# Performance work log

Measured on AMD Instinct MI355X. Metric: run time of the kernel, lower is better.

## Reference

```python
import jax, jax.numpy as jnp
import numpy as np

N, E = 50000, 800000
IN_F, HID_F, OUT_F = 128, 128, 32


def setup_inputs() -> dict:
    key = jax.random.key(0)
    ks = jax.random.split(key, 16)
    glorot = lambda k, i, o: jax.random.normal(k, (i, o), jnp.float32) * (2.0 / (i + o)) ** 0.5
    return {
        "x": jax.random.normal(ks[0], (N, IN_F), jnp.float32),
        "src": jax.random.randint(ks[1], (E,), 0, N, jnp.int64),
        "dst": jax.random.randint(ks[2], (E,), 0, N, jnp.int64),
        # layer 0: mean aggregator
        "W_self0": glorot(ks[3], IN_F, HID_F),
        "W_neigh0": glorot(ks[4], IN_F, HID_F),
        "b0": jnp.zeros((HID_F,), jnp.float32),
        # layers 1,2: gcn aggregator (fc_neigh only)
        "W_neigh1": glorot(ks[5], HID_F, HID_F),
        "b1": jnp.zeros((HID_F,), jnp.float32),
        "W_neigh2": glorot(ks[6], HID_F, HID_F),
        "b2": jnp.zeros((HID_F,), jnp.float32),
        # layer 3: mean aggregator
        "W_self3": glorot(ks[7], HID_F, OUT_F),
        "W_neigh3": glorot(ks[8], HID_F, OUT_F),
        "b3": jnp.zeros((OUT_F,), jnp.float32),
    }


def _l2_normalize(x, eps=1e-12):
    # torch F.normalize(x): x / max(||x||_2, eps) along dim 1
    n = jnp.sqrt(jnp.sum(x * x, axis=1, keepdims=True))
    return x / jnp.maximum(n, eps)


def _agg_sum(h, src, dst, n):
    # sum of in-neighbor (src) features onto dst nodes: [N, d]
    return jax.ops.segment_sum(h[src], dst, num_segments=n)


def _sage_mean(h, src, dst, deg, W_self, W_neigh, b):
    nbr = _agg_sum(h, src, dst, h.shape[0]) / jnp.maximum(deg, 1.0)[:, None]
    return h @ W_self + nbr @ W_neigh + b


def _sage_gcn(h, src, dst, deg, W_neigh, b):
    hn = (_agg_sum(h, src, dst, h.shape[0]) + h) / (deg + 1.0)[:, None]
    return hn @ W_neigh + b


def reference(x, src, dst, W_self0, W_neigh0, b0, W_neigh1, b1, W_neigh2, b2,
              W_self3, W_neigh3, b3):
    n = x.shape[0]
    deg = jax.ops.segment_sum(jnp.ones_like(dst, jnp.float32), dst, num_segments=n)
    h = _l2_normalize(x)
    h = jax.nn.relu(_sage_mean(h, src, dst, deg, W_self0, W_neigh0, b0))
    h = jax.nn.relu(_sage_gcn(h, src, dst, deg, W_neigh1, b1))
    h = jax.nn.relu(_sage_gcn(h, src, dst, deg, W_neigh2, b2))
    h = _sage_mean(h, src, dst, deg, W_self3, W_neigh3, b3)  # no relu on last layer
    return h
```

## Files before the change

kernel.cpp:

```cpp
#include <hip/hip_runtime.h>

#define NN 50000
#define NE 800000
#define F  128
#define FO 32

#define RSH  8
#define RSZ  256
#define NBKT 196
#define CAP  5120
#define PCHUNK 4096
#define NPB  ((NE + PCHUNK - 1) / PCHUNK)
#define LGRID ((NN + 3) / 4)

typedef _Float16 h16;
typedef h16   half8 __attribute__((ext_vector_type(8)));
typedef h16   h16x4 __attribute__((ext_vector_type(4)));
typedef h16   h16x2 __attribute__((ext_vector_type(2)));
typedef float f32x4 __attribute__((ext_vector_type(4)));

__device__ __forceinline__ void wprep_one(const float* __restrict__ W,
        h16* __restrict__ Wf, int idx, int NC, int NCT) {
    if (idx >= 128 * NC) return;
    int k = idx / NC, n = idx - k * NC;
    int kt = k >> 5, g = (k & 31) >> 3, j = k & 7;
    int ct = n >> 4;
    int lane = g * 16 + (n & 15);
    float w = W[idx];
    h16 hi = (h16)w;
    h16 lo = (h16)(w - (float)hi);
    int base = ((kt * NCT + ct) * 64 + lane) * 8 + j;
    Wf[base] = hi;
    Wf[base + NCT * 2048] = lo;
}

__global__ __launch_bounds__(256) void k_pre0(
        const float* __restrict__ S0, const float* __restrict__ N0,
        const float* __restrict__ N1, const float* __restrict__ N2,
        const float* __restrict__ S3, const float* __restrict__ N3,
        h16* fS0, h16* fN0, h16* fN1, h16* fN2, h16* fS3, h16* fN3,
        int* __restrict__ bcur) {
    int bb = blockIdx.x, tid = threadIdx.x;
    if (bb < 256) {
        const float* W = bb < 64 ? S0 : bb < 128 ? N0 : bb < 192 ? N1 : N2;
        h16*        Wf = bb < 64 ? fS0 : bb < 128 ? fN0 : bb < 192 ? fN1 : fN2;
        wprep_one(W, Wf, (bb & 63) * 256 + tid, 128, 8);
    } else if (bb < 288) {
        int b2 = bb - 256;
        const float* W = b2 < 16 ? S3 : N3;
        h16*        Wf = b2 < 16 ? fS3 : fN3;
        wprep_one(W, Wf, (b2 & 15) * 256 + tid, 32, 2);
    } else {
        if (tid < NBKT) bcur[tid] = 0;
    }
}

__global__ __launch_bounds__(256) void k_pre1(const int* __restrict__ src,
        const int* __restrict__ dst, int* __restrict__ bcur, int* __restrict__ barea,
        const float* __restrict__ x, h16* __restrict__ hhi, h16* __restrict__ hlo) {
    __shared__ int cnt[NBKT];
    __shared__ int base[NBKT];
    const int tid = threadIdx.x;
    if ((int)blockIdx.x < NPB) {
        const int e0 = blockIdx.x * PCHUNK;
        for (int i = tid; i < NBKT; i += 256) cnt[i] = 0;
        __syncthreads();
        #pragma unroll
        for (int k = 0; k < PCHUNK / 256; ++k) {
            int e = e0 + k * 256 + tid;
            if (e < NE) atomicAdd(&cnt[dst[e] >> RSH], 1);
        }
        __syncthreads();
        for (int i = tid; i < NBKT; i += 256)
            base[i] = atomicAdd(&bcur[i], cnt[i]);
        __syncthreads();
        for (int i = tid; i < NBKT; i += 256) cnt[i] = base[i];
        __syncthreads();
        #pragma unroll
        for (int k = 0; k < PCHUNK / 256; ++k) {
            int e = e0 + k * 256 + tid;
            if (e < NE) {
                int d = dst[e], s = src[e];
                int b = d >> RSH;
                int p = atomicAdd(&cnt[b], 1);
                barea[b * CAP + p] = ((d & (RSZ - 1)) << 16) | s;
            }
        }
    } else {
        const int bb   = blockIdx.x - NPB;
        const int wid  = bb * 4 + (tid >> 6);
        const int lane = tid & 63;
        if (wid >= NN) return;
        const float2* xr = (const float2*)(x + (size_t)wid * F);
        float2 v = xr[lane];
        float ss = v.x * v.x + v.y * v.y;
        #pragma unroll
        for (int d = 1; d < 64; d <<= 1) ss += __shfl_xor(ss, d, 64);
        float inv = 1.0f / fmaxf(sqrtf(ss), 1e-12f);
        float ox = v.x * inv, oy = v.y * inv;
        h16 hx = (h16)ox, hy = (h16)oy;
        h16x2 vhi = {hx, hy};
        h16x2 vlo = {(h16)(ox - (float)hx), (h16)(oy - (float)hy)};
        *(h16x2*)(hhi + (size_t)wid * F + lane * 2) = vhi;
        *(h16x2*)(hlo + (size_t)wid * F + lane * 2) = vlo;
    }
}

__global__ __launch_bounds__(256) void k_bfill(const int* __restrict__ barea,
        const int* __restrict__ bcur, int* __restrict__ offs,
        float* __restrict__ degf, int* __restrict__ csr) {
    __shared__ int pre[NBKT];
    __shared__ int hist_cur[RSZ];
    __shared__ int ws[4];
    const int r = blockIdx.x, tid = threadIdx.x;
    const int lane = tid & 63, wv = tid >> 6;
    int bv = (tid < NBKT) ? bcur[tid] : 0;
    int bi = bv;
    #pragma unroll
    for (int d = 1; d < 64; d <<= 1) {
        int t = __shfl_up(bi, d, 64);
        if (lane >= d) bi += t;
    }
    if (lane == 63) ws[wv] = bi;
    __syncthreads();
    if (tid == 0) {
        int run = 0;
        #pragma unroll
        for (int w = 0; w < 4; ++w) { int t = ws[w]; ws[w] = run; run += t; }
    }
    __syncthreads();
    if (tid < NBKT) pre[tid] = ws[wv] + bi - bv;
    if (r == 0 && tid == NBKT - 1) offs[NN] = ws[wv] + bi;
    __syncthreads();
    const int nb    = bcur[r];
    const int gbase = pre[r];
    const int node  = (r << RSH) + tid;
    hist_cur[tid] = 0;
    __syncthreads();
    const int* area = barea + r * CAP;
    for (int i = tid; i < nb; i += 256) atomicAdd(&hist_cur[area[i] >> 16], 1);
    __syncthreads();
    const int v = hist_cur[tid];
    int incl = v;
    #pragma unroll
    for (int d = 1; d < 64; d <<= 1) {
        int t = __shfl_up(incl, d, 64);
        if (lane >= d) incl += t;
    }
    __syncthreads();
    if (lane == 63) ws[wv] = incl;
    __syncthreads();
    if (tid == 0) {
        int run = 0;
        #pragma unroll
        for (int w = 0; w < 4; ++w) { int t = ws[w]; ws[w] = run; run += t; }
    }
    __syncthreads();
    const int ex = ws[wv] + incl - v;
    if (node < NN) {
        offs[node] = gbase + ex;
        degf[node] = (float)v;
    }
    __syncthreads();
    hist_cur[tid] = gbase + ex;
    __syncthreads();
    for (int i = tid; i < nb; i += 256) {
        int pk = area[i];
        int p = atomicAdd(&hist_cur[pk >> 16], 1);
        csr[p] = pk & 0xFFFF;
    }
}

template<int NCT, bool OUT16>
__device__ __forceinline__ void mfma_cols(const half8* Ahi, const half8* Alo,
        const h16* __restrict__ Wf, void* __restrict__ out, int row0, int l) {
    const int cdc = l & 15;
    const int cdr = (l >> 4) * 4;
    #pragma unroll
    for (int ct = 0; ct < NCT; ++ct) {
        f32x4 acc = {0.f, 0.f, 0.f, 0.f};
        #pragma unroll
        for (int kt = 0; kt < 4; ++kt) {
            half8 bh = *(const half8*)(Wf + (size_t)(((kt * NCT + ct) * 64 + l) * 8));
            half8 bl = *(const half8*)(Wf + (size_t)((((4 + kt) * NCT + ct) * 64 + l) * 8));
            acc = __builtin_amdgcn_mfma_f32_16x16x32_f16(Ahi[kt], bh, acc, 0, 0, 0);
            acc = __builtin_amdgcn_mfma_f32_16x16x32_f16(Alo[kt], bh, acc, 0, 0, 0);
            acc = __builtin_amdgcn_mfma_f32_16x16x32_f16(Ahi[kt], bl, acc, 0, 0, 0);
        }
        #pragma unroll
        for (int r = 0; r < 4; ++r) {
            int gr = row0 + cdr + r;
            if (gr < NN) {
                size_t oi = (size_t)gr * (NCT * 16) + ct * 16 + cdc;
                if constexpr (OUT16) ((h16*)out)[oi] = (h16)acc[r];
                else                 ((float*)out)[oi] = acc[r];
            }
        }
    }
}

template<int NCTA, int NCTB, bool A16, bool B16>
__global__ __launch_bounds__(256) void k_mfma(const h16* __restrict__ hhi,
        const h16* __restrict__ hlo, const h16* __restrict__ WfA,
        const h16* __restrict__ WfB, void* __restrict__ outA,
        void* __restrict__ outB) {
    const int tid = threadIdx.x;
    const int l   = tid & 63;
    const int wv  = tid >> 6;
    const int row0 = blockIdx.x * 64 + wv * 16;
    int ar = row0 + (l & 15); if (ar >= NN) ar = NN - 1;
    const size_t ab = (size_t)ar * F + (l >> 4) * 8;
    half8 Ahi[4], Alo[4];
    #pragma unroll
    for (int kt = 0; kt < 4; ++kt) {
        Ahi[kt] = *(const half8*)(hhi + ab + kt * 32);
        Alo[kt] = *(const half8*)(hlo + ab + kt * 32);
    }
    mfma_cols<NCTA, A16>(Ahi, Alo, WfA, outA, row0, l);
    if constexpr (NCTB > 0) mfma_cols<NCTB, B16>(Ahi, Alo, WfB, outB, row0, l);
}

template<int MODE>
__global__ __launch_bounds__(256) void k_agg128(const h16* __restrict__ g,
        const h16* __restrict__ s, const int* __restrict__ offs,
        const int* __restrict__ csr, const float* __restrict__ degf,
        const float* __restrict__ b, h16* __restrict__ hhi, h16* __restrict__ hlo) {
    const int wid  = (int)((blockIdx.x * 256 + threadIdx.x) >> 6);
    const int lane = threadIdx.x & 63;
    if (wid >= NN) return;
    const int q  = lane >> 4;
    const int li = lane & 15;
    const int beg = offs[wid], end = offs[wid + 1];
    const half8* g8 = (const half8*)g;
    float a0[8], a1[8];
    #pragma unroll
    for (int j = 0; j < 8; ++j) { a0[j] = 0.f; a1[j] = 0.f; }
    int e = beg;
    for (; e + 16 <= end; e += 16) {
        int u0 = csr[e + q];
        int u1 = csr[e + 4 + q];
        int u2 = csr[e + 8 + q];
        int u3 = csr[e + 12 + q];
        half8 v0 = g8[(size_t)u0 * 16 + li];
        half8 v1 = g8[(size_t)u1 * 16 + li];
        half8 v2 = g8[(size_t)u2 * 16 + li];
        half8 v3 = g8[(size_t)u3 * 16 + li];
        #pragma unroll
        for (int j = 0; j < 8; ++j) {
            a0[j] += (float)v0[j] + (float)v2[j];
            a1[j] += (float)v1[j] + (float)v3[j];
        }
    }
    for (; e + 4 <= end; e += 4) {
        half8 v = g8[(size_t)csr[e + q] * 16 + li];
        #pragma unroll
        for (int j = 0; j < 8; ++j) a0[j] += (float)v[j];
    }
    if (q < end - e) {
        half8 v = g8[(size_t)csr[e + q] * 16 + li];
        #pragma unroll
        for (int j = 0; j < 8; ++j) a1[j] += (float)v[j];
    }
    #pragma unroll
    for (int j = 0; j < 8; ++j) {
        a0[j] += a1[j];
        a0[j] += __shfl_xor(a0[j], 16, 64);
        a0[j] += __shfl_xor(a0[j], 32, 64);
    }
    if (q) return;
    const float dg = degf[wid];
    float bb[8];
    *(float4*)(bb)     = *(const float4*)(b + li * 8);
    *(float4*)(bb + 4) = *(const float4*)(b + li * 8 + 4);
    float r[8];
    if (MODE == 0) {
        float inv = 1.f / fmaxf(dg, 1.f);
        half8 sv = ((const half8*)s)[(size_t)wid * 16 + li];
        #pragma unroll
        for (int j = 0; j < 8; ++j)
            r[j] = fmaxf((float)sv[j] + a0[j] * inv + bb[j], 0.f);
    } else {
        float inv = 1.f / (dg + 1.f);
        half8 gv = g8[(size_t)wid * 16 + li];
        #pragma unroll
        for (int j = 0; j < 8; ++j)
            r[j] = fmaxf((a0[j] + (float)gv[j]) * inv + bb[j], 0.f);
    }
    half8 vhi, vlo;
    #pragma unroll
    for (int j = 0; j < 8; ++j) {
        h16 hi = (h16)r[j];
        vhi[j] = hi;
        vlo[j] = (h16)(r[j] - (float)hi);
    }
    *(half8*)(hhi + (size_t)wid * F + li * 8) = vhi;
    *(half8*)(hlo + (size_t)wid * F + li * 8) = vlo;
}

__global__ __launch_bounds__(256) void k_agg32(const h16* __restrict__ g,
        const h16* __restrict__ s, const int* __restrict__ offs,
        const int* __restrict__ csr, const float* __restrict__ degf,
        const float* __restrict__ b, float* __restrict__ out) {
    const int wid  = (int)((blockIdx.x * 256 + threadIdx.x) >> 6);
    const int lane = threadIdx.x & 63;
    if (wid >= NN) return;
    const int grp = lane >> 3;
    const int li  = lane & 7;
    const int beg = offs[wid], end = offs[wid + 1];
    const h16x4* g4 = (const h16x4*)g;
    float a0[4] = {0.f, 0.f, 0.f, 0.f}, a1[4] = {0.f, 0.f, 0.f, 0.f};
    int e = beg + grp;
    for (; e + 8 < end; e += 16) {
        int u0 = csr[e], u1 = csr[e + 8];
        h16x4 v0 = g4[(size_t)u0 * 8 + li];
        h16x4 v1 = g4[(size_t)u1 * 8 + li];
        #pragma unroll
        for (int j = 0; j < 4; ++j) { a0[j] += (float)v0[j]; a1[j] += (float)v1[j]; }
    }
    if (e < end) {
        h16x4 v = g4[(size_t)csr[e] * 8 + li];
        #pragma unroll
        for (int j = 0; j < 4; ++j) a0[j] += (float)v[j];
    }
    #pragma unroll
    for (int j = 0; j < 4; ++j) {
        a0[j] += a1[j];
        a0[j] += __shfl_xor(a0[j], 8, 64);
        a0[j] += __shfl_xor(a0[j], 16, 64);
        a0[j] += __shfl_xor(a0[j], 32, 64);
    }
    if (grp) return;
    const float inv = 1.f / fmaxf(degf[wid], 1.f);
    float4 bb = ((const float4*)b)[li];
    h16x4 sv = ((const h16x4*)s)[(size_t)wid * 8 + li];
    float4 r;
    r.x = (float)sv[0] + a0[0] * inv + bb.x;
    r.y = (float)sv[1] + a0[1] * inv + bb.y;
    r.z = (float)sv[2] + a0[2] * inv + bb.z;
    r.w = (float)sv[3] + a0[3] * inv + bb.w;
    ((float4*)out)[(size_t)wid * 8 + li] = r;
}

extern "C" void kernel_launch(void* const* d_in, const int* in_sizes, int n_in,
                              void* d_out, int out_size, void* d_ws, size_t ws_size,
                              hipStream_t stream) {
    const float* x       = (const float*)d_in[0];
    const int*   src     = (const int*)  d_in[1];
    const int*   dst     = (const int*)  d_in[2];
    const float* Wself0  = (const float*)d_in[3];
    const float* Wneigh0 = (const float*)d_in[4];
    const float* b0      = (const float*)d_in[5];
    const float* Wneigh1 = (const float*)d_in[6];
    const float* b1      = (const float*)d_in[7];
    const float* Wneigh2 = (const float*)d_in[8];
    const float* b2      = (const float*)d_in[9];
    const float* Wself3  = (const float*)d_in[10];
    const float* Wneigh3 = (const float*)d_in[11];
    const float* b3      = (const float*)d_in[12];
    float* out = (float*)d_out;

    char* ws = (char*)d_ws;
    size_t off = 0;
    auto alloc = [&](size_t bytes) -> void* {
        void* p = ws + off;
        off += (bytes + 255) & ~(size_t)255;
        return p;
    };
    float* degf   = (float*)alloc((size_t)NN * 4);
    int*   offs   = (int*)  alloc((size_t)(NN + 1) * 4);
    int*   csr    = (int*)  alloc((size_t)NE * 4);
    int*   bcur   = (int*)  alloc((size_t)NBKT * 4);
    int*   barea  = (int*)  alloc((size_t)NBKT * CAP * 4);
    h16*   hhi    = (h16*)  alloc((size_t)NN * F * 2);
    h16*   hlo    = (h16*)  alloc((size_t)NN * F * 2);
    h16*   gh     = (h16*)  alloc((size_t)NN * F * 2);
    h16*   s16    = (h16*)  alloc((size_t)NN * F * 2);
    h16*   WfS0   = (h16*)  alloc((size_t)128 * 128 * 2 * 2);
    h16*   WfN0   = (h16*)  alloc((size_t)128 * 128 * 2 * 2);
    h16*   WfN1   = (h16*)  alloc((size_t)128 * 128 * 2 * 2);
    h16*   WfN2   = (h16*)  alloc((size_t)128 * 128 * 2 * 2);
    h16*   WfS3   = (h16*)  alloc((size_t)128 * 32 * 2 * 2);
    h16*   WfN3   = (h16*)  alloc((size_t)128 * 32 * 2 * 2);

    const int mgrid = (NN + 63) / 64;

    k_pre0<<<289, 256, 0, stream>>>(Wself0, Wneigh0, Wneigh1, Wneigh2,
                                    Wself3, Wneigh3,
                                    WfS0, WfN0, WfN1, WfN2, WfS3, WfN3, bcur);
    k_pre1<<<NPB + LGRID, 256, 0, stream>>>(src, dst, bcur, barea, x, hhi, hlo);
    k_bfill<<<NBKT, 256, 0, stream>>>(barea, bcur, offs, degf, csr);

    k_mfma<8, 8, true, true><<<mgrid, 256, 0, stream>>>(hhi, hlo, WfS0, WfN0, s16, gh);
    k_agg128<0><<<LGRID, 256, 0, stream>>>(gh, s16, offs, csr, degf, b0, hhi, hlo);

    k_mfma<8, 0, true, false><<<mgrid, 256, 0, stream>>>(hhi, hlo, WfN1, nullptr, gh, nullptr);
    k_agg128<1><<<LGRID, 256, 0, stream>>>(gh, nullptr, offs, csr, degf, b1, hhi, hlo);

    k_mfma<8, 0, true, false><<<mgrid, 256, 0, stream>>>(hhi, hlo, WfN2, nullptr, gh, nullptr);
    k_agg128<1><<<LGRID, 256, 0, stream>>>(gh, nullptr, offs, csr, degf, b2, hhi, hlo);

    k_mfma<2, 2, true, true><<<mgrid, 256, 0, stream>>>(hhi, hlo, WfS3, WfN3, s16, gh);
    k_agg32<<<LGRID, 256, 0, stream>>>(gh, s16, offs, csr, degf, b3, out);
}
```

Before: 313.7 us.

## Fuse neighbor aggregation with next layer's MFMA matmul via LDS staging

Each layer's aggregation kernel now writes its activated hi/lo fp16 rows into shared memory, and the same block immediately runs the next layer's MFMA transform. This removes the hhi/hlo round trip through global memory and several kernel launches. The L2-normalize step is likewise fused with the first-layer matmul inside k_pre1. The trade-off is less latency hiding: each wave now aggregates 16 nodes serially, so the grid is 4x smaller, and each block uses more shared memory.

Result: slower. 326.3 us (+4.0%).

```diff
diff --git a/kernel.cpp b/kernel.cpp
--- a/kernel.cpp
+++ b/kernel.cpp
@@ -11,6 +11,7 @@
 #define CAP  5120
 #define PCHUNK 4096
 #define NPB  ((NE + PCHUNK - 1) / PCHUNK)
+#define MG   ((NN + 63) / 64)
 #define LGRID ((NN + 3) / 4)
 
 typedef _Float16 h16;
@@ -55,13 +56,176 @@
     }
 }
 
+template<int NCT>
+__device__ __forceinline__ void mfma_cols(const half8* Ahi, const half8* Alo,
+        const h16* __restrict__ Wf, h16* __restrict__ out, int row0, int l) {
+    const int cdc = l & 15;
+    const int cdr = (l >> 4) * 4;
+    #pragma unroll
+    for (int ct = 0; ct < NCT; ++ct) {
+        f32x4 acc = {0.f, 0.f, 0.f, 0.f};
+        #pragma unroll
+        for (int kt = 0; kt < 4; ++kt) {
+            half8 bh = *(const half8*)(Wf + (size_t)(((kt * NCT + ct) * 64 + l) * 8));
+            half8 bl = *(const half8*)(Wf + (size_t)((((4 + kt) * NCT + ct) * 64 + l) * 8));
+            acc = __builtin_amdgcn_mfma_f32_16x16x32_f16(Ahi[kt], bh, acc, 0, 0, 0);
+            acc = __builtin_amdgcn_mfma_f32_16x16x32_f16(Alo[kt], bh, acc, 0, 0, 0);
+            acc = __builtin_amdgcn_mfma_f32_16x16x32_f16(Ahi[kt], bl, acc, 0, 0, 0);
+        }
+        #pragma unroll
+        for (int r = 0; r < 4; ++r) {
+            int gr = row0 + cdr + r;
+            if (gr < NN) out[(size_t)gr * (NCT * 16) + ct * 16 + cdc] = (h16)acc[r];
+        }
+    }
+}
+
+template<int NCTA, int NCTB, int MODE>
+__device__ __forceinline__ void fused_body(int blk, int tid,
+        h16* __restrict__ AhiW, h16* __restrict__ AloW,
+        const h16* __restrict__ g, const h16* __restrict__ s,
+        const float* __restrict__ x,
+        const int* __restrict__ offs, const int* __restrict__ csr,
+        const float* __restrict__ degf, const float* __restrict__ bias,
+        const h16* __restrict__ WfA, const h16* __restrict__ WfB,
+        h16* __restrict__ outA, h16* __restrict__ outB) {
+    const int l  = tid & 63;
+    const int wv = tid >> 6;
+    const int row0 = blk * 64 + wv * 16;
+
+    if constexpr (MODE == 2) {
+        #pragma unroll 1
+        for (int i = 0; i < 16; ++i) {
+            int nd = row0 + i;
+            float ox = 0.f, oy = 0.f;
+            if (nd < NN) {
+                float2 v = ((const float2*)(x + (size_t)nd * F))[l];
+                float ss = v.x * v.x + v.y * v.y;
+                #pragma unroll
+                for (int d = 1; d < 64; d <<= 1) ss += __shfl_xor(ss, d, 64);
+                float inv = 1.0f / fmaxf(sqrtf(ss), 1e-12f);
+                ox = v.x * inv; oy = v.y * inv;
+            }
+            h16 hx = (h16)ox, hy = (h16)oy;
+            h16x2 vhi = {hx, hy};
+            h16x2 vlo = {(h16)(ox - (float)hx), (h16)(oy - (float)hy)};
+            *(h16x2*)(AhiW + i * 136 + l * 2) = vhi;
+            *(h16x2*)(AloW + i * 136 + l * 2) = vlo;
+        }
+    } else {
+        const int q  = l >> 4;
+        const int li = l & 15;
+        const half8* g8 = (const half8*)g;
+        #pragma unroll 1
+        for (int i = 0; i < 16; ++i) {
+            int nd = row0 + i;
+            float r[8] = {0.f, 0.f, 0.f, 0.f, 0.f, 0.f, 0.f, 0.f};
+            if (nd < NN) {
+                const int beg = offs[nd], end = offs[nd + 1];
+                float a0[8], a1[8];
+                #pragma unroll
+                for (int j = 0; j < 8; ++j) { a0[j] = 0.f; a1[j] = 0.f; }
+                int e = beg;
+                for (; e + 16 <= end; e += 16) {
+                    int u0 = csr[e + q];
+                    int u1 = csr[e + 4 + q];
+                    int u2 = csr[e + 8 + q];
+                    int u3 = csr[e + 12 + q];
+                    half8 v0 = g8[(size_t)u0 * 16 + li];
+                    half8 v1 = g8[(size_t)u1 * 16 + li];
+                    half8 v2 = g8[(size_t)u2 * 16 + li];
+                    half8 v3 = g8[(size_t)u3 * 16 + li];
+                    #pragma unroll
+                    for (int j = 0; j < 8; ++j) {
+                        a0[j] += (float)v0[j] + (float)v2[j];
+                        a1[j] += (float)v1[j] + (float)v3[j];
+                    }
+                }
+                for (; e + 4 <= end; e += 4) {
+                    half8 v = g8[(size_t)csr[e + q] * 16 + li];
+                    #pragma unroll
+                    for (int j = 0; j < 8; ++j) a0[j] += (float)v[j];
+                }
+                if (q < end - e) {
+                    half8 v = g8[(size_t)csr[e + q] * 16 + li];
+                    #pragma unroll
+                    for (int j = 0; j < 8; ++j) a1[j] += (float)v[j];
+                }
+                #pragma unroll
+                for (int j = 0; j < 8; ++j) {
+                    a0[j] += a1[j];
+                    a0[j] += __shfl_xor(a0[j], 16, 64);
+                    a0[j] += __shfl_xor(a0[j], 32, 64);
+                }
+                const float dg = degf[nd];
+                float bb[8];
+                *(float4*)(bb)     = *(const float4*)(bias + li * 8);
+                *(float4*)(bb + 4) = *(const float4*)(bias + li * 8 + 4);
+                if constexpr (MODE == 0) {
+                    float inv = 1.f / fmaxf(dg, 1.f);
+                    half8 sv = ((const half8*)s)[(size_t)nd * 16 + li];
+                    #pragma unroll
+                    for (int j = 0; j < 8; ++j)
+                        r[j] = fmaxf((float)sv[j] + a0[j] * inv + bb[j], 0.f);
+                } else {
+                    float inv = 1.f / (dg + 1.f);
+                    half8 gv = g8[(size_t)nd * 16 + li];
+                    #pragma unroll
+                    for (int j = 0; j < 8; ++j)
+                        r[j] = fmaxf((a0[j] + (float)gv[j]) * inv + bb[j], 0.f);
+                }
+            }
+            if (q == 0) {
+                half8 vhi, vlo;
+                #pragma unroll
+                for (int j = 0; j < 8; ++j) {
+                    h16 hi = (h16)r[j];
+                    vhi[j] = hi;
+                    vlo[j] = (h16)(r[j] - (float)hi);
+                }
+                *(half8*)(AhiW + i * 136 + li * 8) = vhi;
+                *(half8*)(AloW + i * 136 + li * 8) = vlo;
+            }
+        }
+    }
+
+    half8 Ahi[4], Alo[4];
+    const h16* ah = AhiW + (l & 15) * 136 + (l >> 4) * 8;
+    const h16* al = AloW + (l & 15) * 136 + (l >> 4) * 8;
+    #pragma unroll
+    for (int kt = 0; kt < 4; ++kt) {
+        Ahi[kt] = *(const half8*)(ah + kt * 32);
+        Alo[kt] = *(const half8*)(al + kt * 32);
+    }
+    mfma_cols<NCTA>(Ahi, Alo, WfA, outA, row0, l);
+    if constexpr (NCTB > 0) mfma_cols<NCTB>(Ahi, Alo, WfB, outB, row0, l);
+}
+
+template<int NCTA, int NCTB, int MODE>
+__global__ __launch_bounds__(256) void k_fused(
+        const h16* __restrict__ g, const h16* __restrict__ s,
+        const int* __restrict__ offs, const int* __restrict__ csr,
+        const float* __restrict__ degf, const float* __restrict__ bias,
+        const h16* __restrict__ WfA, const h16* __restrict__ WfB,
+        h16* __restrict__ outA, h16* __restrict__ outB) {
+    __shared__ h16 Ah[4][16][136];
+    __shared__ h16 Al[4][16][136];
+    const int wv = threadIdx.x >> 6;
+    fused_body<NCTA, NCTB, MODE>(blockIdx.x, threadIdx.x,
+        &Ah[wv][0][0], &Al[wv][0][0], g, s, nullptr,
+        offs, csr, degf, bias, WfA, WfB, outA, outB);
+}
+
 __global__ __launch_bounds__(256) void k_pre1(const int* __restrict__ src,
         const int* __restrict__ dst, int* __restrict__ bcur, int* __restrict__ barea,
-        const float* __restrict__ x, h16* __restrict__ hhi, h16* __restrict__ hlo) {
-    __shared__ int cnt[NBKT];
-    __shared__ int base[NBKT];
+        const float* __restrict__ x, const h16* __restrict__ WfS0,
+        const h16* __restrict__ WfN0, h16* __restrict__ s16, h16* __restrict__ gh) {
+    __shared__ h16 Ah[4][16][136];
+    __shared__ h16 Al[4][16][136];
     const int tid = threadIdx.x;
     if ((int)blockIdx.x < NPB) {
+        int* cnt  = (int*)&Ah[0][0][0];
+        int* base = cnt + NBKT;
         const int e0 = blockIdx.x * PCHUNK;
         for (int i = tid; i < NBKT; i += 256) cnt[i] = 0;
         __syncthreads();
@@ -80,29 +244,17 @@
         for (int k = 0; k < PCHUNK / 256; ++k) {
             int e = e0 + k * 256 + tid;
             if (e < NE) {
-                int d = dst[e], s = src[e];
+                int d = dst[e], sv = src[e];
                 int b = d >> RSH;
                 int p = atomicAdd(&cnt[b], 1);
-                barea[b * CAP + p] = ((d & (RSZ - 1)) << 16) | s;
+                barea[b * CAP + p] = ((d & (RSZ - 1)) << 16) | sv;
             }
         }
     } else {
-        const int bb   = blockIdx.x - NPB;
-        const int wid  = bb * 4 + (tid >> 6);
-        const int lane = tid & 63;
-        if (wid >= NN) return;
-        const float2* xr = (const float2*)(x + (size_t)wid * F);
-        float2 v = xr[lane];
-        float ss = v.x * v.x + v.y * v.y;
-        #pragma unroll
-        for (int d = 1; d < 64; d <<= 1) ss += __shfl_xor(ss, d, 64);
-        float inv = 1.0f / fmaxf(sqrtf(ss), 1e-12f);
-        float ox = v.x * inv, oy = v.y * inv;
-        h16 hx = (h16)ox, hy = (h16)oy;
-        h16x2 vhi = {hx, hy};
-        h16x2 vlo = {(h16)(ox - (float)hx), (h16)(oy - (float)hy)};
-        *(h16x2*)(hhi + (size_t)wid * F + lane * 2) = vhi;
-        *(h16x2*)(hlo + (size_t)wid * F + lane * 2) = vlo;
+        const int wv = tid >> 6;
+        fused_body<8, 8, 2>((int)blockIdx.x - NPB, tid,
+            &Ah[wv][0][0], &Al[wv][0][0], nullptr, nullptr, x,
+            nullptr, nullptr, nullptr, nullptr, WfS0, WfN0, s16, gh);
     }
 }
 
@@ -169,132 +321,6 @@
         int p = atomicAdd(&hist_cur[pk >> 16], 1);
         csr[p] = pk & 0xFFFF;
     }
-}
-
-template<int NCT, bool OUT16>
-__device__ __forceinline__ void mfma_cols(const half8* Ahi, const half8* Alo,
-        const h16* __restrict__ Wf, void* __restrict__ out, int row0, int l) {
-    const int cdc = l & 15;
-    const int cdr = (l >> 4) * 4;
-    #pragma unroll
-    for (int ct = 0; ct < NCT; ++ct) {
-        f32x4 acc = {0.f, 0.f, 0.f, 0.f};
-        #pragma unroll
-        for (int kt = 0; kt < 4; ++kt) {
-            half8 bh = *(const half8*)(Wf + (size_t)(((kt * NCT + ct) * 64 + l) * 8));
-            half8 bl = *(const half8*)(Wf + (size_t)((((4 + kt) * NCT + ct) * 64 + l) * 8));
-            acc = __builtin_amdgcn_mfma_f32_16x16x32_f16(Ahi[kt], bh, acc, 0, 0, 0);
-            acc = __builtin_amdgcn_mfma_f32_16x16x32_f16(Alo[kt], bh, acc, 0, 0, 0);
-            acc = __builtin_amdgcn_mfma_f32_16x16x32_f16(Ahi[kt], bl, acc, 0, 0, 0);
-        }
-        #pragma unroll
-        for (int r = 0; r < 4; ++r) {
-            int gr = row0 + cdr + r;
-            if (gr < NN) {
-                size_t oi = (size_t)gr * (NCT * 16) + ct * 16 + cdc;
-                if constexpr (OUT16) ((h16*)out)[oi] = (h16)acc[r];
-                else                 ((float*)out)[oi] = acc[r];
-            }
-        }
-    }
-}
-
-template<int NCTA, int NCTB, bool A16, bool B16>
-__global__ __launch_bounds__(256) void k_mfma(const h16* __restrict__ hhi,
-        const h16* __restrict__ hlo, const h16* __restrict__ WfA,
-        const h16* __restrict__ WfB, void* __restrict__ outA,
-        void* __restrict__ outB) {
-    const int tid = threadIdx.x;
-    const int l   = tid & 63;
-    const int wv  = tid >> 6;
-    const int row0 = blockIdx.x * 64 + wv * 16;
-    int ar = row0 + (l & 15); if (ar >= NN) ar = NN - 1;
-    const size_t ab = (size_t)ar * F + (l >> 4) * 8;
-    half8 Ahi[4], Alo[4];
-    #pragma unroll
-    for (int kt = 0; kt < 4; ++kt) {
-        Ahi[kt] = *(const half8*)(hhi + ab + kt * 32);
-        Alo[kt] = *(const half8*)(hlo + ab + kt * 32);
-    }
-    mfma_cols<NCTA, A16>(Ahi, Alo, WfA, outA, row0, l);
-    if constexpr (NCTB > 0) mfma_cols<NCTB, B16>(Ahi, Alo, WfB, outB, row0, l);
-}
-
-template<int MODE>
-__global__ __launch_bounds__(256) void k_agg128(const h16* __restrict__ g,
-        const h16* __restrict__ s, const int* __restrict__ offs,
-        const int* __restrict__ csr, const float* __restrict__ degf,
-        const float* __restrict__ b, h16* __restrict__ hhi, h16* __restrict__ hlo) {
-    const int wid  = (int)((blockIdx.x * 256 + threadIdx.x) >> 6);
-    const int lane = threadIdx.x & 63;
-    if (wid >= NN) return;
-    const int q  = lane >> 4;
-    const int li = lane & 15;
-    const int beg = offs[wid], end = offs[wid + 1];
-    const half8* g8 = (const half8*)g;
-    float a0[8], a1[8];
-    #pragma unroll
-    for (int j = 0; j < 8; ++j) { a0[j] = 0.f; a1[j] = 0.f; }
-    int e = beg;
-    for (; e + 16 <= end; e += 16) {
-        int u0 = csr[e + q];
-        int u1 = csr[e + 4 + q];
-        int u2 = csr[e + 8 + q];
-        int u3 = csr[e + 12 + q];
-        half8 v0 = g8[(size_t)u0 * 16 + li];
-        half8 v1 = g8[(size_t)u1 * 16 + li];
-        half8 v2 = g8[(size_t)u2 * 16 + li];
-        half8 v3 = g8[(size_t)u3 * 16 + li];
-        #pragma unroll
-        for (int j = 0; j < 8; ++j) {
-            a0[j] += (float)v0[j] + (float)v2[j];
-            a1[j] += (float)v1[j] + (float)v3[j];
-        }
-    }
-    for (; e + 4 <= end; e += 4) {
-        half8 v = g8[(size_t)csr[e + q] * 16 + li];
-        #pragma unroll
-        for (int j = 0; j < 8; ++j) a0[j] += (float)v[j];
-    }
-    if (q < end - e) {
-        half8 v = g8[(size_t)csr[e + q] * 16 + li];
-        #pragma unroll
-        for (int j = 0; j < 8; ++j) a1[j] += (float)v[j];
-    }
-    #pragma unroll
-    for (int j = 0; j < 8; ++j) {
-        a0[j] += a1[j];
-        a0[j] += __shfl_xor(a0[j], 16, 64);
-        a0[j] += __shfl_xor(a0[j], 32, 64);
-    }
-    if (q) return;
-    const float dg = degf[wid];
-    float bb[8];
-    *(float4*)(bb)     = *(const float4*)(b + li * 8);
-    *(float4*)(bb + 4) = *(const float4*)(b + li * 8 + 4);
-    float r[8];
-    if (MODE == 0) {
-        float inv = 1.f / fmaxf(dg, 1.f);
-        half8 sv = ((const half8*)s)[(size_t)wid * 16 + li];
-        #pragma unroll
-        for (int j = 0; j < 8; ++j)
-            r[j] = fmaxf((float)sv[j] + a0[j] * inv + bb[j], 0.f);
-    } else {
-        float inv = 1.f / (dg + 1.f);
-        half8 gv = g8[(size_t)wid * 16 + li];
-        #pragma unroll
-        for (int j = 0; j < 8; ++j)
-            r[j] = fmaxf((a0[j] + (float)gv[j]) * inv + bb[j], 0.f);
-    }
-    half8 vhi, vlo;
-    #pragma unroll
-    for (int j = 0; j < 8; ++j) {
-        h16 hi = (h16)r[j];
-        vhi[j] = hi;
-        vlo[j] = (h16)(r[j] - (float)hi);
-    }
-    *(half8*)(hhi + (size_t)wid * F + li * 8) = vhi;
-    *(half8*)(hlo + (size_t)wid * F + li * 8) = vlo;
 }
 
 __global__ __launch_bounds__(256) void k_agg32(const h16* __restrict__ g,
@@ -371,10 +397,11 @@
     int*   csr    = (int*)  alloc((size_t)NE * 4);
     int*   bcur   = (int*)  alloc((size_t)NBKT * 4);
     int*   barea  = (int*)  alloc((size_t)NBKT * CAP * 4);
-    h16*   hhi    = (h16*)  alloc((size_t)NN * F * 2);
-    h16*   hlo    = (h16*)  alloc((size_t)NN * F * 2);
-    h16*   gh     = (h16*)  alloc((size_t)NN * F * 2);
     h16*   s16    = (h16*)  alloc((size_t)NN * F * 2);
+    h16*   ghA    = (h16*)  alloc((size_t)NN * F * 2);
+    h16*   ghB    = (h16*)  alloc((size_t)NN * F * 2);
+    h16*   s16b   = (h16*)  alloc((size_t)NN * FO * 2);
+    h16*   gh4    = (h16*)  alloc((size_t)NN * FO * 2);
     h16*   WfS0   = (h16*)  alloc((size_t)128 * 128 * 2 * 2);
     h16*   WfN0   = (h16*)  alloc((size_t)128 * 128 * 2 * 2);
     h16*   WfN1   = (h16*)  alloc((size_t)128 * 128 * 2 * 2);
@@ -382,23 +409,18 @@
     h16*   WfS3   = (h16*)  alloc((size_t)128 * 32 * 2 * 2);
     h16*   WfN3   = (h16*)  alloc((size_t)128 * 32 * 2 * 2);
 
-    const int mgrid = (NN + 63) / 64;
-
     k_pre0<<<289, 256, 0, stream>>>(Wself0, Wneigh0, Wneigh1, Wneigh2,
                                     Wself3, Wneigh3,
                                     WfS0, WfN0, WfN1, WfN2, WfS3, WfN3, bcur);
-    k_pre1<<<NPB + LGRID, 256, 0, stream>>>(src, dst, bcur, barea, x, hhi, hlo);
+    k_pre1<<<NPB + MG, 256, 0, stream>>>(src, dst, bcur, barea, x,
+                                         WfS0, WfN0, s16, ghA);
     k_bfill<<<NBKT, 256, 0, stream>>>(barea, bcur, offs, degf, csr);
 
-    k_mfma<8, 8, true, true><<<mgrid, 256, 0, stream>>>(hhi, hlo, WfS0, WfN0, s16, gh);
-    k_agg128<0><<<LGRID, 256, 0, stream>>>(gh, s16, offs, csr, degf, b0, hhi, hlo);
-
-    k_mfma<8, 0, true, false><<<mgrid, 256, 0, stream>>>(hhi, hlo, WfN1, nullptr, gh, nullptr);
-    k_agg128<1><<<LGRID, 256, 0, stream>>>(gh, nullptr, offs, csr, degf, b1, hhi, hlo);
-
-    k_mfma<8, 0, true, false><<<mgrid, 256, 0, stream>>>(hhi, hlo, WfN2, nullptr, gh, nullptr);
-    k_agg128<1><<<LGRID, 256, 0, stream>>>(gh, nullptr, offs, csr, degf, b2, hhi, hlo);
-
-    k_mfma<2, 2, true, true><<<mgrid, 256, 0, stream>>>(hhi, hlo, WfS3, WfN3, s16, gh);
-    k_agg32<<<LGRID, 256, 0, stream>>>(gh, s16, offs, csr, degf, b3, out);
-}
+    k_fused<8, 0, 0><<<MG, 256, 0, stream>>>(ghA, s16, offs, csr, degf, b0,
+                                             WfN1, nullptr, ghB, nullptr);
+    k_fused<8, 0, 1><<<MG, 256, 0, stream>>>(ghB, nullptr, offs, csr, degf, b1,
+                                             WfN2, nullptr, ghA, nullptr);
+    k_fused<2, 2, 1><<<MG, 256, 0, stream>>>(ghA, nullptr, offs, csr, degf, b2,
+                                             WfS3, WfN3, s16b, gh4);
+    k_agg32<<<LGRID, 256, 0, stream>>>(gh4, s16b, offs, csr, degf, b3, out);
+}
```

## Pad CSR rows to multiples of 16 with dummy node and fuse bfill with first GEMM

Applied to the files above, without the earlier changes.

Each node's CSR neighbour list is padded to a multiple of 16 entries. The padding points at a zeroed sentinel row NN, so the aggregation kernels run only full 16-wide gather iterations with no tail loops. Buckets get a fixed stride (CAP16), which removes the global prefix scan, and the bucket-fill work is merged into the same launch as the layer-0 MFMA GEMM. This saves a kernel launch and lets the two jobs overlap, at the cost of extra padded gathers and a larger CSR buffer, and it assumes no bucket holds more than CAP16 padded entries.

New measurement: 297.0 us. 5.3% less time.

```diff
diff --git a/kernel.cpp b/kernel.cpp
--- a/kernel.cpp
+++ b/kernel.cpp
@@ -9,8 +9,10 @@
 #define RSZ  256
 #define NBKT 196
 #define CAP  5120
+#define CAP16 9216
 #define PCHUNK 4096
 #define NPB  ((NE + PCHUNK - 1) / PCHUNK)
+#define MG   ((NN + 63) / 64)
 #define LGRID ((NN + 3) / 4)
 
 typedef _Float16 h16;
@@ -39,7 +41,8 @@
         const float* __restrict__ N1, const float* __restrict__ N2,
         const float* __restrict__ S3, const float* __restrict__ N3,
         h16* fS0, h16* fN0, h16* fN1, h16* fN2, h16* fS3, h16* fN3,
-        int* __restrict__ bcur) {
+        int* __restrict__ bcur, h16* __restrict__ ghA, h16* __restrict__ ghB,
+        h16* __restrict__ gh4) {
     int bb = blockIdx.x, tid = threadIdx.x;
     if (bb < 256) {
         const float* W = bb < 64 ? S0 : bb < 128 ? N0 : bb < 192 ? N1 : N2;
@@ -52,6 +55,11 @@
         wprep_one(W, Wf, (b2 & 15) * 256 + tid, 32, 2);
     } else {
         if (tid < NBKT) bcur[tid] = 0;
+        if (tid < F) {
+            ghA[(size_t)NN * F + tid] = (h16)0.f;
+            ghB[(size_t)NN * F + tid] = (h16)0.f;
+        }
+        if (tid < FO) gh4[(size_t)NN * FO + tid] = (h16)0.f;
     }
 }
 
@@ -80,10 +88,10 @@
         for (int k = 0; k < PCHUNK / 256; ++k) {
             int e = e0 + k * 256 + tid;
             if (e < NE) {
-                int d = dst[e], s = src[e];
+                int d = dst[e], sv = src[e];
                 int b = d >> RSH;
                 int p = atomicAdd(&cnt[b], 1);
-                barea[b * CAP + p] = ((d & (RSZ - 1)) << 16) | s;
+                barea[b * CAP + p] = ((d & (RSZ - 1)) << 16) | sv;
             }
         }
     } else {
@@ -106,71 +114,6 @@
     }
 }
 
-__global__ __launch_bounds__(256) void k_bfill(const int* __restrict__ barea,
-        const int* __restrict__ bcur, int* __restrict__ offs,
-        float* __restrict__ degf, int* __restrict__ csr) {
-    __shared__ int pre[NBKT];
-    __shared__ int hist_cur[RSZ];
-    __shared__ int ws[4];
-    const int r = blockIdx.x, tid = threadIdx.x;
-    const int lane = tid & 63, wv = tid >> 6;
-    int bv = (tid < NBKT) ? bcur[tid] : 0;
-    int bi = bv;
-    #pragma unroll
-    for (int d = 1; d < 64; d <<= 1) {
-        int t = __shfl_up(bi, d, 64);
-        if (lane >= d) bi += t;
-    }
-    if (lane == 63) ws[wv] = bi;
-    __syncthreads();
-    if (tid == 0) {
-        int run = 0;
-        #pragma unroll
-        for (int w = 0; w < 4; ++w) { int t = ws[w]; ws[w] = run; run += t; }
-    }
-    __syncthreads();
-    if (tid < NBKT) pre[tid] = ws[wv] + bi - bv;
-    if (r == 0 && tid == NBKT - 1) offs[NN] = ws[wv] + bi;
-    __syncthreads();
-    const int nb    = bcur[r];
-    const int gbase = pre[r];
-    const int node  = (r << RSH) + tid;
-    hist_cur[tid] = 0;
-    __syncthreads();
-    const int* area = barea + r * CAP;
-    for (int i = tid; i < nb; i += 256) atomicAdd(&hist_cur[area[i] >> 16], 1);
-    __syncthreads();
-    const int v = hist_cur[tid];
-    int incl = v;
-    #pragma unroll
-    for (int d = 1; d < 64; d <<= 1) {
-        int t = __shfl_up(incl, d, 64);
-        if (lane >= d) incl += t;
-    }
-    __syncthreads();
-    if (lane == 63) ws[wv] = incl;
-    __syncthreads();
-    if (tid == 0) {
-        int run = 0;
-        #pragma unroll
-        for (int w = 0; w < 4; ++w) { int t = ws[w]; ws[w] = run; run += t; }
-    }
-    __syncthreads();
-    const int ex = ws[wv] + incl - v;
-    if (node < NN) {
-        offs[node] = gbase + ex;
-        degf[node] = (float)v;
-    }
-    __syncthreads();
-    hist_cur[tid] = gbase + ex;
-    __syncthreads();
-    for (int i = tid; i < nb; i += 256) {
-        int pk = area[i];
-        int p = atomicAdd(&hist_cur[pk >> 16], 1);
-        csr[p] = pk & 0xFFFF;
-    }
-}
-
 template<int NCT, bool OUT16>
 __device__ __forceinline__ void mfma_cols(const half8* Ahi, const half8* Alo,
         const h16* __restrict__ Wf, void* __restrict__ out, int row0, int l) {
@@ -199,15 +142,14 @@
     }
 }
 
-template<int NCTA, int NCTB, bool A16, bool B16>
-__global__ __launch_bounds__(256) void k_mfma(const h16* __restrict__ hhi,
-        const h16* __restrict__ hlo, const h16* __restrict__ WfA,
-        const h16* __restrict__ WfB, void* __restrict__ outA,
-        void* __restrict__ outB) {
-    const int tid = threadIdx.x;
-    const int l   = tid & 63;
-    const int wv  = tid >> 6;
-    const int row0 = blockIdx.x * 64 + wv * 16;
+template<int NCTA, int NCTB>
+__device__ __forceinline__ void mfma_block(int blk, int tid,
+        const h16* __restrict__ hhi, const h16* __restrict__ hlo,
+        const h16* __restrict__ WfA, const h16* __restrict__ WfB,
+        h16* __restrict__ outA, h16* __restrict__ outB) {
+    const int l  = tid & 63;
+    const int wv = tid >> 6;
+    const int row0 = blk * 64 + wv * 16;
     int ar = row0 + (l & 15); if (ar >= NN) ar = NN - 1;
     const size_t ab = (size_t)ar * F + (l >> 4) * 8;
     half8 Ahi[4], Alo[4];
@@ -216,8 +158,70 @@
         Ahi[kt] = *(const half8*)(hhi + ab + kt * 32);
         Alo[kt] = *(const half8*)(hlo + ab + kt * 32);
     }
-    mfma_cols<NCTA, A16>(Ahi, Alo, WfA, outA, row0, l);
-    if constexpr (NCTB > 0) mfma_cols<NCTB, B16>(Ahi, Alo, WfB, outB, row0, l);
+    mfma_cols<NCTA, true>(Ahi, Alo, WfA, (void*)outA, row0, l);
+    if constexpr (NCTB > 0) mfma_cols<NCTB, true>(Ahi, Alo, WfB, (void*)outB, row0, l);
+}
+
+template<int NCTA, int NCTB>
+__global__ __launch_bounds__(256) void k_mfma(const h16* __restrict__ hhi,
+        const h16* __restrict__ hlo, const h16* __restrict__ WfA,
+        const h16* __restrict__ WfB, h16* __restrict__ outA,
+        h16* __restrict__ outB) {
+    mfma_block<NCTA, NCTB>(blockIdx.x, threadIdx.x, hhi, hlo, WfA, WfB, outA, outB);
+}
+
+__global__ __launch_bounds__(256) void k_bfill_mfma(
+        const int* __restrict__ barea, const int* __restrict__ bcur,
+        int* __restrict__ offs, float* __restrict__ degf, int* __restrict__ csr,
+        const h16* __restrict__ hhi, const h16* __restrict__ hlo,
+        const h16* __restrict__ WfA, const h16* __restrict__ WfB,
+        h16* __restrict__ outA, h16* __restrict__ outB) {
+    __shared__ int hist[RSZ];
+    __shared__ int ws[4];
+    const int tid = threadIdx.x;
+    if ((int)blockIdx.x < NBKT) {
+        const int r = blockIdx.x;
+        const int lane = tid & 63, wv = tid >> 6;
+        const int nb = bcur[r];
+        hist[tid] = 0;
+        __syncthreads();
+        const int* area = barea + r * CAP;
+        for (int i = tid; i < nb; i += 256) atomicAdd(&hist[area[i] >> 16], 1);
+        __syncthreads();
+        const int v   = hist[tid];
+        const int psz = (v + 15) & ~15;
+        int incl = psz;
+        #pragma unroll
+        for (int d = 1; d < 64; d <<= 1) {
+            int t = __shfl_up(incl, d, 64);
+            if (lane >= d) incl += t;
+        }
+        if (lane == 63) ws[wv] = incl;
+        __syncthreads();
+        if (tid == 0) {
+            int run = 0;
+            #pragma unroll
+            for (int w = 0; w < 4; ++w) { int t = ws[w]; ws[w] = run; run += t; }
+        }
+        __syncthreads();
+        const int beg  = r * CAP16 + ws[wv] + incl - psz;
+        const int node = (r << RSH) + tid;
+        if (node < NN) {
+            offs[node] = beg;
+            degf[node] = (float)v;
+        }
+        __syncthreads();
+        hist[tid] = beg;
+        __syncthreads();
+        for (int i = tid; i < nb; i += 256) {
+            int pk = area[i];
+            int p = atomicAdd(&hist[pk >> 16], 1);
+            csr[p] = pk & 0xFFFF;
+        }
+        for (int i = v; i < psz; ++i) csr[beg + i] = NN;
+    } else {
+        mfma_block<8, 8>((int)blockIdx.x - NBKT, tid, hhi, hlo, WfA, WfB, outA, outB);
+    }
 }
 
 template<int MODE>
@@ -230,13 +234,15 @@
     if (wid >= NN) return;
     const int q  = lane >> 4;
     const int li = lane & 15;
-    const int beg = offs[wid], end = offs[wid + 1];
+    const int beg = offs[wid];
+    const float dgf = degf[wid];
+    const int n16 = ((int)dgf + 15) >> 4;
     const half8* g8 = (const half8*)g;
     float a0[8], a1[8];
     #pragma unroll
     for (int j = 0; j < 8; ++j) { a0[j] = 0.f; a1[j] = 0.f; }
-    int e = beg;
-    for (; e + 16 <= end; e += 16) {
+    for (int t = 0; t < n16; ++t) {
+        const int e = beg + (t << 4);
         int u0 = csr[e + q];
         int u1 = csr[e + 4 + q];
         int u2 = csr[e + 8 + q];
@@ -251,16 +257,6 @@
             a1[j] += (float)v1[j] + (float)v3[j];
         }
     }
-    for (; e + 4 <= end; e += 4) {
-        half8 v = g8[(size_t)csr[e + q] * 16 + li];
-        #pragma unroll
-        for (int j = 0; j < 8; ++j) a0[j] += (float)v[j];
-    }
-    if (q < end - e) {
-        half8 v = g8[(size_t)csr[e + q] * 16 + li];
-        #pragma unroll
-        for (int j = 0; j < 8; ++j) a1[j] += (float)v[j];
-    }
     #pragma unroll
     for (int j = 0; j < 8; ++j) {
         a0[j] += a1[j];
@@ -268,19 +264,18 @@
         a0[j] += __shfl_xor(a0[j], 32, 64);
     }
     if (q) return;
-    const float dg = degf[wid];
     float bb[8];
     *(float4*)(bb)     = *(const float4*)(b + li * 8);
     *(float4*)(bb + 4) = *(const float4*)(b + li * 8 + 4);
     float r[8];
     if (MODE == 0) {
-        float inv = 1.f / fmaxf(dg, 1.f);
+        float inv = 1.f / fmaxf(dgf, 1.f);
         half8 sv = ((const half8*)s)[(size_t)wid * 16 + li];
         #pragma unroll
         for (int j = 0; j < 8; ++j)
             r[j] = fmaxf((float)sv[j] + a0[j] * inv + bb[j], 0.f);
     } else {
-        float inv = 1.f / (dg + 1.f);
+        float inv = 1.f / (dgf + 1.f);
         half8 gv = g8[(size_t)wid * 16 + li];
         #pragma unroll
         for (int j = 0; j < 8; ++j)
@@ -306,21 +301,18 @@
     if (wid >= NN) return;
     const int grp = lane >> 3;
     const int li  = lane & 7;
-    const int beg = offs[wid], end = offs[wid + 1];
+    const int beg = offs[wid];
+    const float dgf = degf[wid];
+    const int n16 = ((int)dgf + 15) >> 4;
     const h16x4* g4 = (const h16x4*)g;
     float a0[4] = {0.f, 0.f, 0.f, 0.f}, a1[4] = {0.f, 0.f, 0.f, 0.f};
-    int e = beg + grp;
-    for (; e + 8 < end; e += 16) {
-        int u0 = csr[e], u1 = csr[e + 8];
+    for (int t = 0; t < n16; ++t) {
+        const int e = beg + (t << 4);
+        int u0 = csr[e + grp], u1 = csr[e + 8 + grp];
         h16x4 v0 = g4[(size_t)u0 * 8 + li];
         h16x4 v1 = g4[(size_t)u1 * 8 + li];
         #pragma unroll
         for (int j = 0; j < 4; ++j) { a0[j] += (float)v0[j]; a1[j] += (float)v1[j]; }
-    }
-    if (e < end) {
-        h16x4 v = g4[(size_t)csr[e] * 8 + li];
-        #pragma unroll
-        for (int j = 0; j < 4; ++j) a0[j] += (float)v[j];
     }
     #pragma unroll
     for (int j = 0; j < 4; ++j) {
@@ -330,7 +322,7 @@
         a0[j] += __shfl_xor(a0[j], 32, 64);
     }
     if (grp) return;
-    const float inv = 1.f / fmaxf(degf[wid], 1.f);
+    const float inv = 1.f / fmaxf(dgf, 1.f);
     float4 bb = ((const float4*)b)[li];
     h16x4 sv = ((const h16x4*)s)[(size_t)wid * 8 + li];
     float4 r;
@@ -368,13 +360,16 @@
     };
     float* degf   = (float*)alloc((size_t)NN * 4);
     int*   offs   = (int*)  alloc((size_t)(NN + 1) * 4);
-    int*   csr    = (int*)  alloc((size_t)NE * 4);
+    int*   csr    = (int*)  alloc((size_t)NBKT * CAP16 * 4);
     int*   bcur   = (int*)  alloc((size_t)NBKT * 4);
     int*   barea  = (int*)  alloc((size_t)NBKT * CAP * 4);
     h16*   hhi    = (h16*)  alloc((size_t)NN * F * 2);
     h16*   hlo    = (h16*)  alloc((size_t)NN * F * 2);
-    h16*   gh     = (h16*)  alloc((size_t)NN * F * 2);
     h16*   s16    = (h16*)  alloc((size_t)NN * F * 2);
+    h16*   ghA    = (h16*)  alloc((size_t)(NN + 1) * F * 2);
+    h16*   ghB    = (h16*)  alloc((size_t)(NN + 1) * F * 2);
+    h16*   s16b   = (h16*)  alloc((size_t)NN * FO * 2);
+    h16*   gh4    = (h16*)  alloc((size_t)(NN + 1) * FO * 2);
     h16*   WfS0   = (h16*)  alloc((size_t)128 * 128 * 2 * 2);
     h16*   WfN0   = (h16*)  alloc((size_t)128 * 128 * 2 * 2);
     h16*   WfN1   = (h16*)  alloc((size_t)128 * 128 * 2 * 2);
@@ -382,23 +377,18 @@
     h16*   WfS3   = (h16*)  alloc((size_t)128 * 32 * 2 * 2);
     h16*   WfN3   = (h16*)  alloc((size_t)128 * 32 * 2 * 2);
 
-    const int mgrid = (NN + 63) / 64;
-
     k_pre0<<<289, 256, 0, stream>>>(Wself0, Wneigh0, Wneigh1, Wneigh2,
                                     Wself3, Wneigh3,
-                                    WfS0, WfN0, WfN1, WfN2, WfS3, WfN3, bcur);
+                                    WfS0, WfN0, WfN1, WfN2, WfS3, WfN3,
+                                    bcur, ghA, ghB, gh4);
     k_pre1<<<NPB + LGRID, 256, 0, stream>>>(src, dst, bcur, barea, x, hhi, hlo);
-    k_bfill<<<NBKT, 256, 0, stream>>>(barea, bcur, offs, degf, csr);
-
-    k_mfma<8, 8, true, true><<<mgrid, 256, 0, stream>>>(hhi, hlo, WfS0, WfN0, s16, gh);
-    k_agg128<0><<<LGRID, 256, 0, stream>>>(gh, s16, offs, csr, degf, b0, hhi, hlo);
-
-    k_mfma<8, 0, true, false><<<mgrid, 256, 0, stream>>>(hhi, hlo, WfN1, nullptr, gh, nullptr);
-    k_agg128<1><<<LGRID, 256, 0, stream>>>(gh, nullptr, offs, csr, degf, b1, hhi, hlo);
-
-    k_mfma<8, 0, true, false><<<mgrid, 256, 0, stream>>>(hhi, hlo, WfN2, nullptr, gh, nullptr);
-    k_agg128<1><<<LGRID, 256, 0, stream>>>(gh, nullptr, offs, csr, degf, b2, hhi, hlo);
-
-    k_mfma<2, 2, true, true><<<mgrid, 256, 0, stream>>>(hhi, hlo, WfS3, WfN3, s16, gh);
-    k_agg32<<<LGRID, 256, 0, stream>>>(gh, s16, offs, csr, degf, b3, out);
-}
+    k_bfill_mfma<<<NBKT + MG, 256, 0, stream>>>(barea, bcur, offs, degf, csr,
+                                                hhi, hlo, WfS0, WfN0, s16, ghA);
+    k_agg128<0><<<LGRID, 256, 0, stream>>>(ghA, s16, offs, csr, degf, b0, hhi, hlo);
+    k_mfma<8, 0><<<MG, 256, 0, stream>>>(hhi, hlo, WfN1, nullptr, ghB, nullptr);
+    k_agg128<1><<<LGRID, 256, 0, stream>>>(ghB, nullptr, offs, csr, degf, b1, hhi, hlo);
+    k_mfma<8, 0><<<MG, 256, 0, stream>>>(hhi, hlo, WfN2, nullptr, ghA, nullptr);
+    k_agg128<1><<<LGRID, 256, 0, stream>>>(ghA, nullptr, offs, csr, degf, b2, hhi, hlo);
+    k_mfma<2, 2><<<MG, 256, 0, stream>>>(hhi, hlo, WfS3, WfN3, s16b, gh4);
+    k_agg32<<<LGRID, 256, 0, stream>>>(gh4, s16b, offs, csr, degf, b3, out);
+}
```
